# Kernel tuning notes

Measured on AMD Instinct MI355X. Metric: run time of the kernel, lower is better.

The kernel has to match this reference:

```python
import jax, jax.numpy as jnp
import numpy as np

SCALES = jnp.asarray([0.5, 1.0, 2.0], dtype=jnp.float32)  # distance_scales
GROUP_THRESHOLD = 2.0
EPS = 1e-6


def _pairwise_norm(x):
    # x: (B, T, N, 2) -> (B, T, N, N) euclidean distances, diagonal == 0
    diff = x[:, :, :, None, :] - x[:, :, None, :, :]
    sq = jnp.sum(diff * diff, axis=-1)
    safe = jnp.where(sq > 0, sq, 1.0)
    return jnp.where(sq > 0, jnp.sqrt(safe), 0.0)


def _assign_groups_one(d_last, threshold):
    # d_last: (N, N) pairwise distances at last timestep.
    # Sequential greedy grouping (faithful to the torch loop) via lax.scan over agents.
    N = d_last.shape[0]
    idx = jnp.arange(N)

    def step(carry, i):
        assigned, groups, cur = carry
        is_new = jnp.logical_not(assigned[i])  # agent i starts a new group
        # i itself (dist 0) plus unassigned j > i within threshold
        newly = is_new & jnp.logical_not(assigned) & (d_last[i] <= threshold) & (idx >= i)
        groups = jnp.where(newly, cur, groups)
        assigned = assigned | newly
        cur = cur + is_new.astype(jnp.int32)
        return (assigned, groups, cur), None

    init = (jnp.zeros(N, dtype=bool), jnp.zeros(N, dtype=jnp.int32), jnp.int32(0))
    (_, groups, _), _ = jax.lax.scan(step, init, idx)
    return groups


def setup_inputs() -> dict:
    key = jax.random.key(0)
    k1, k2 = jax.random.split(key)
    B, T, N = 8, 16, 256
    positions = jax.random.uniform(k1, (B, T, N, 2), dtype=jnp.float32) * 20.0
    displacements = jax.random.normal(k2, (B, T, N, 2), dtype=jnp.float32)
    return {"positions": positions, "displacements": displacements}


def reference(positions, displacements):
    # positions, displacements: (B, T, N, 2)
    pairwise_dist = _pairwise_norm(positions)       # (B, T, N, N)
    pairwise_disp = _pairwise_norm(displacements)   # (B, T, N, N)

    # build_relations: (B, R, T, N, N)
    dist_adj = (pairwise_dist[:, None] <= SCALES.reshape(1, -1, 1, 1, 1)).astype(pairwise_dist.dtype)
    disp_w = 1.0 / (pairwise_disp + EPS)
    disp_w = jnp.where(jnp.isinf(disp_w), 0.0, disp_w)
    adjacency = dist_adj * disp_w[:, None]

    # group assignment from last-timestep positions
    d_last = pairwise_dist[:, -1]  # (B, N, N)
    group_indices = jax.vmap(lambda d: _assign_groups_one(d, GROUP_THRESHOLD))(d_last)  # (B, N)

    # intra-group masking
    gmask = (group_indices[:, :, None] == group_indices[:, None, :]).astype(adjacency.dtype)  # (B, N, N)
    intra_adjacency = adjacency * gmask[:, None, None]

    return adjacency, group_indices, intra_adjacency
```

## Files before the change

kernel.cpp:

```cpp
#include <hip/hip_runtime.h>

#define NB 8
#define NT 16
#define NN 256
#define NS 3

typedef float f32x4 __attribute__((ext_vector_type(4)));
typedef int   i32x4 __attribute__((ext_vector_type(4)));

__global__ __launch_bounds__(64) void groups_kernel(
    const float* __restrict__ positions,
    float* __restrict__ out_groups_f,
    int* __restrict__ out_groups_i)
{
    const int b    = blockIdx.x;
    const int lane = threadIdx.x;

    const float2* __restrict__ P =
        ((const float2*)positions) + ((size_t)b * NT + (NT - 1)) * NN;

    float px[4], py[4];
#pragma unroll
    for (int k = 0; k < 4; ++k) {
        const float2 p = P[k * 64 + lane];
        px[k] = p.x; py[k] = p.y;
    }

    unsigned long long amask[4] = {0ull, 0ull, 0ull, 0ull};
    int grp[4] = {0, 0, 0, 0};
    int cur = 0;

#pragma unroll
    for (int ki = 0; ki < 4; ++ki) {
        for (int li = 0; li < 64; ++li) {
            if ((amask[ki] >> li) & 1ull) continue;
            const float pix = __shfl(px[ki], li);
            const float piy = __shfl(py[ki], li);
#pragma unroll
            for (int k = ki; k < 4; ++k) {
                const bool elig = (k > ki) || (lane >= li);
                const bool unas = (((amask[k] >> lane) & 1ull) == 0ull);
                const float dx = pix - px[k];
                const float dy = piy - py[k];
                const float sq = __fadd_rn(__fmul_rn(dx, dx), __fmul_rn(dy, dy));
                const float d  = (sq > 0.0f) ? __fsqrt_rn(sq) : 0.0f;
                const bool newly = elig && unas && (d <= 2.0f);
                const unsigned long long nb = __ballot(newly);
                amask[k] |= nb;
                if (newly) grp[k] = cur;
            }
            ++cur;
            if (!(~(amask[0] & amask[1] & amask[2] & amask[3]))) break;
        }
    }

#pragma unroll
    for (int k = 0; k < 4; ++k) {
        const int j = b * NN + k * 64 + lane;
        out_groups_i[j] = grp[k];
        out_groups_f[j] = (float)grp[k];
    }
}

#define CHUNKS 8
#define ROWS (NN / CHUNKS)

__global__ __launch_bounds__(NN) void adj_kernel(
    const float* __restrict__ positions,
    const float* __restrict__ displacements,
    const int* __restrict__ groups,
    float* __restrict__ adj,
    float* __restrict__ intra)
{
    __shared__ float px[NN], py[NN], ux[NN], uy[NN];
    __shared__ int grp[NN];

    const int blk = blockIdx.x;
    const int c   = blk & 7;
    const int bt  = blk >> 3;
    const int t   = bt & 15;
    const int b   = bt >> 4;
    const int tid = threadIdx.x;

    {
        const float2 p = ((const float2*)positions)[((size_t)b * NT + t) * NN + tid];
        const float2 u = ((const float2*)displacements)[((size_t)b * NT + t) * NN + tid];
        px[tid] = p.x;  py[tid] = p.y;
        ux[tid] = u.x;  uy[tid] = u.y;
        grp[tid] = groups[b * NN + tid];
    }
    __syncthreads();

    const int cl = tid & 63;
    const int rw = tid >> 6;

    const f32x4 pxj = ((const f32x4*)px)[cl];
    const f32x4 pyj = ((const f32x4*)py)[cl];
    const f32x4 uxj = ((const f32x4*)ux)[cl];
    const f32x4 uyj = ((const f32x4*)uy)[cl];
    const i32x4 gj  = ((const i32x4*)grp)[cl];

    const size_t splane  = (size_t)NT * NN * NN;
    const size_t base_bt = ((size_t)(b * NS) * NT + t) * (size_t)(NN * NN);

    for (int q = 0; q < ROWS / 4; ++q) {
        const int i = c * ROWS + q * 4 + rw;
        const float pix = px[i], piy = py[i];
        const float uix = ux[i], uiy = uy[i];
        const int   gi  = grp[i];

        f32x4 A0, A1, A2, I0, I1, I2;

#pragma unroll
        for (int cc = 0; cc < 4; ++cc) {
            const float dx = pix - pxj[cc];
            const float dy = piy - pyj[cc];
            const float sq = __fadd_rn(__fmul_rn(dx, dx), __fmul_rn(dy, dy));
            const float d  = (sq > 0.0f) ? __fsqrt_rn(sq) : 0.0f;

            const float ex = uix - uxj[cc];
            const float ey = uiy - uyj[cc];
            const float sqe = __fadd_rn(__fmul_rn(ex, ex), __fmul_rn(ey, ey));
            const float dn  = __builtin_amdgcn_sqrtf(sqe);
            const float w   = __builtin_amdgcn_rcpf(dn + 1e-6f);

            const float gm = (gi == gj[cc]) ? 1.0f : 0.0f;
            const float a0 = (d <= 0.5f) ? w : 0.0f;
            const float a1 = (d <= 1.0f) ? w : 0.0f;
            const float a2 = (d <= 2.0f) ? w : 0.0f;

            A0[cc] = a0;       A1[cc] = a1;       A2[cc] = a2;
            I0[cc] = a0 * gm;  I1[cc] = a1 * gm;  I2[cc] = a2 * gm;
        }

        const size_t off = base_bt + (size_t)i * NN + 4 * cl;
        *(f32x4*)(adj + off)                = A0;
        *(f32x4*)(adj + off + splane)       = A1;
        *(f32x4*)(adj + off + 2 * splane)   = A2;
        *(f32x4*)(intra + off)              = I0;
        *(f32x4*)(intra + off + splane)     = I1;
        *(f32x4*)(intra + off + 2 * splane) = I2;
    }
}

extern "C" void kernel_launch(void* const* d_in, const int* in_sizes, int n_in,
                              void* d_out, int out_size, void* d_ws, size_t ws_size,
                              hipStream_t stream) {
    const float* positions     = (const float*)d_in[0];
    const float* displacements = (const float*)d_in[1];
    float* out = (float*)d_out;

    const size_t ADJ_ELEMS = (size_t)NB * NS * NT * NN * NN;
    float* adj      = out;
    float* groups_f = out + ADJ_ELEMS;
    float* intra    = out + ADJ_ELEMS + (size_t)NB * NN;
    int*   groups_i = (int*)d_ws;

    groups_kernel<<<NB, 64, 0, stream>>>(positions, groups_f, groups_i);
    adj_kernel<<<NB * NT * CHUNKS, NN, 0, stream>>>(positions, displacements,
                                                    groups_i, adj, intra);
}
```

Baseline: 218.5 us.

## Give each adjacency block one contiguous output plane instead of six strided ones

The adjacency kernel used to have each block write six separate planes (three scales, adj and intra) for a row chunk. Now each block writes one contiguous half-plane for a single (output, batch, scale, timestep), so stores from a block stay in one region and hit DRAM more sequentially. The grid grows from 1024 to 1536 blocks. The pairwise math is recomputed for every scale and output, so ALU work goes up about sixfold in exchange for a simpler write pattern. It also drops the sq>0 guard before the sqrt.

Result: no change. 220.9 us (+1.1%).

```diff
diff --git a/kernel.cpp b/kernel.cpp
--- a/kernel.cpp
+++ b/kernel.cpp
@@ -62,10 +62,9 @@
     }
 }
 
-#define CHUNKS 8
-#define ROWS (NN / CHUNKS)
+#define PLANE_BLOCKS (NB * NS * NT * 2)
 
-__global__ __launch_bounds__(NN) void adj_kernel(
+__global__ __launch_bounds__(256) void adj_kernel(
     const float* __restrict__ positions,
     const float* __restrict__ displacements,
     const int* __restrict__ groups,
@@ -75,12 +74,15 @@
     __shared__ float px[NN], py[NN], ux[NN], uy[NN];
     __shared__ int grp[NN];
 
-    const int blk = blockIdx.x;
-    const int c   = blk & 7;
-    const int bt  = blk >> 3;
-    const int t   = bt & 15;
-    const int b   = bt >> 4;
-    const int tid = threadIdx.x;
+    const int n       = blockIdx.x;
+    const int isIntra = (n >= PLANE_BLOCKS) ? 1 : 0;
+    const int slab    = isIntra ? (n - PLANE_BLOCKS) : n;
+    const int half    = slab & 1;
+    const int t       = (slab >> 1) & 15;
+    const int bs      = slab >> 5;
+    const int s       = bs % 3;
+    const int b       = bs / 3;
+    const int tid     = threadIdx.x;
 
     {
         const float2 p = ((const float2*)positions)[((size_t)b * NT + t) * NN + tid];
@@ -100,23 +102,25 @@
     const f32x4 uyj = ((const f32x4*)uy)[cl];
     const i32x4 gj  = ((const i32x4*)grp)[cl];
 
-    const size_t splane  = (size_t)NT * NN * NN;
-    const size_t base_bt = ((size_t)(b * NS) * NT + t) * (size_t)(NN * NN);
+    const float S = (s == 0) ? 0.5f : ((s == 1) ? 1.0f : 2.0f);
+    float* __restrict__ outp =
+        (isIntra ? intra : adj) + ((size_t)bs * NT + t) * (size_t)(NN * NN);
 
-    for (int q = 0; q < ROWS / 4; ++q) {
-        const int i = c * ROWS + q * 4 + rw;
+    const int r0 = half * 128 + rw * 32;
+
+    for (int q = 0; q < 32; ++q) {
+        const int i = r0 + q;
         const float pix = px[i], piy = py[i];
         const float uix = ux[i], uiy = uy[i];
         const int   gi  = grp[i];
 
-        f32x4 A0, A1, A2, I0, I1, I2;
-
+        f32x4 V;
 #pragma unroll
         for (int cc = 0; cc < 4; ++cc) {
             const float dx = pix - pxj[cc];
             const float dy = piy - pyj[cc];
             const float sq = __fadd_rn(__fmul_rn(dx, dx), __fmul_rn(dy, dy));
-            const float d  = (sq > 0.0f) ? __fsqrt_rn(sq) : 0.0f;
+            const float d  = __fsqrt_rn(sq);
 
             const float ex = uix - uxj[cc];
             const float ey = uiy - uyj[cc];
@@ -124,22 +128,12 @@
             const float dn  = __builtin_amdgcn_sqrtf(sqe);
             const float w   = __builtin_amdgcn_rcpf(dn + 1e-6f);
 
-            const float gm = (gi == gj[cc]) ? 1.0f : 0.0f;
-            const float a0 = (d <= 0.5f) ? w : 0.0f;
-            const float a1 = (d <= 1.0f) ? w : 0.0f;
-            const float a2 = (d <= 2.0f) ? w : 0.0f;
-
-            A0[cc] = a0;       A1[cc] = a1;       A2[cc] = a2;
-            I0[cc] = a0 * gm;  I1[cc] = a1 * gm;  I2[cc] = a2 * gm;
+            const float gmv = (gi == gj[cc]) ? 1.0f : 0.0f;
+            const float fac = isIntra ? gmv : 1.0f;
+            V[cc] = (d <= S) ? w * fac : 0.0f;
         }
 
-        const size_t off = base_bt + (size_t)i * NN + 4 * cl;
-        *(f32x4*)(adj + off)                = A0;
-        *(f32x4*)(adj + off + splane)       = A1;
-        *(f32x4*)(adj + off + 2 * splane)   = A2;
-        *(f32x4*)(intra + off)              = I0;
-        *(f32x4*)(intra + off + splane)     = I1;
-        *(f32x4*)(intra + off + 2 * splane) = I2;
+        *(f32x4*)(outp + (size_t)i * NN + 4 * cl) = V;
     }
 }
 
@@ -157,6 +151,6 @@
     int*   groups_i = (int*)d_ws;
 
     groups_kernel<<<NB, 64, 0, stream>>>(positions, groups_f, groups_i);
-    adj_kernel<<<NB * NT * CHUNKS, NN, 0, stream>>>(positions, displacements,
-                                                    groups_i, adj, intra);
+    adj_kernel<<<2 * PLANE_BLOCKS, 256, 0, stream>>>(positions, displacements,
+                                                     groups_i, adj, intra);
 }
```
